# Kernel optimization log

Hardware: AMD Instinct MI355X
Metric: run time of the kernel (lower is better)

Reference implementation:

```python
import jax, jax.numpy as jnp
import numpy as np

N, T, F_IN, F_OUT, E = 20000, 4, 64, 64, 640000


def setup_inputs() -> dict:
    key = jax.random.key(0)
    k1, k2, k3, k4, k5, k6 = jax.random.split(key, 6)
    node_features = jax.random.normal(k1, (N, T, F_IN), dtype=jnp.float32)
    edge_weights = jax.random.uniform(k2, (T, E), dtype=jnp.float32)
    src = jax.random.randint(k3, (E,), 0, N, dtype=jnp.int32)
    dst = jax.random.randint(k4, (E,), 0, N, dtype=jnp.int32)
    W = jax.random.normal(k5, (F_OUT, F_IN), dtype=jnp.float32) / np.sqrt(F_IN)
    b = jax.random.normal(k6, (F_OUT,), dtype=jnp.float32) * 0.01
    return {"node_features": node_features, "edge_weights": edge_weights,
            "src": src, "dst": dst, "W": W, "b": b}


def reference(node_features, edge_weights, src, dst, W, b):
    # u_mul_e: gather source node features and scale by per-edge, per-time weight
    # edge_weights (T, E) -> transposed (E, T) -> broadcast over feature dim
    msg = node_features[src] * edge_weights.T[:, :, None]          # (E, T, F_IN)
    # fn.sum: scatter-sum messages into destination nodes
    h = jax.ops.segment_sum(msg, dst, num_segments=node_features.shape[0])  # (N, T, F_IN)
    # nn.Linear(in_features, out_features)
    return h @ W.T + b                                             # (N, T, F_OUT)
```

## Files before the change

kernel.cpp:

```cpp
#include <hip/hip_runtime.h>

#define N_NODES 20000
#define T_STEPS 4
#define F_DIM   64
#define E_EDGES 640000
#define ROWS    (N_NODES * T_STEPS)
#define ROW_ELEMS (T_STEPS * F_DIM)

#define SCATTER_BLOCKS   (E_EDGES / 1024)
#define TRANSFORM_BLOCKS (ROWS / 64)
#define OVF_CAP          4096

__device__ __forceinline__ unsigned short f32_to_bf16_rne(float f) {
    unsigned u = __float_as_uint(f);
    u += 0x7FFFu + ((u >> 16) & 1u);
    return (unsigned short)(u >> 16);
}
__device__ __forceinline__ float bf16_to_f32(unsigned short h) {
    return __uint_as_float((unsigned)h << 16);
}
__device__ __forceinline__ unsigned w_to_u12(float f) {
    unsigned q = __float2uint_rn(f * 4096.0f);
    return q > 4095u ? 4095u : q;
}

__global__ __launch_bounds__(256) void fused_build_kernel(
    const float* __restrict__ x, const float* __restrict__ W,
    unsigned short* __restrict__ yb,
    const int* __restrict__ src, const int* __restrict__ dst,
    const float* __restrict__ ew,
    int* __restrict__ cnt, uint2* __restrict__ buckets, int cap,
    int4* __restrict__ ovf, int* __restrict__ ovf_cnt)
{
    __shared__ float wt[64 * 64];

    if (blockIdx.x < SCATTER_BLOCKS) {
        const int base = blockIdx.x * 1024 + threadIdx.x;
#pragma unroll
        for (int j = 0; j < 4; ++j) {
            const int e = base + j * 256;
            const unsigned w0 = w_to_u12(ew[e]);
            const unsigned w1 = w_to_u12(ew[E_EDGES + e]);
            const unsigned w2 = w_to_u12(ew[2 * E_EDGES + e]);
            const unsigned w3 = w_to_u12(ew[3 * E_EDGES + e]);
            const unsigned s  = (unsigned)src[e];
            const unsigned lo = s | (w0 << 16) | (w1 << 28);
            const unsigned hi = (w1 >> 4) | (w2 << 8) | (w3 << 20);
            const int d = dst[e];
            const int pos = atomicAdd(&cnt[d], 1);
            if (pos < cap) {
                buckets[(size_t)d * cap + pos] = make_uint2(lo, hi);
            } else {
                const int o = atomicAdd(ovf_cnt, 1);
                if (o < OVF_CAP) { int4 r; r.x = (int)lo; r.y = (int)hi; r.z = d; r.w = 0; ovf[o] = r; }
            }
        }
        return;
    }

    const int tid  = threadIdx.x;
    const int row0 = (blockIdx.x - SCATTER_BLOCKS) * 64;

    {
        const int o  = tid & 63;
        const int fb = (tid >> 6) * 16;
#pragma unroll
        for (int k = 0; k < 16; ++k) {
            const int f = fb + k;
            wt[f * 64 + o] = W[o * 64 + f];
        }
    }
    __syncthreads();

    const int rg = tid >> 4;
    const int oq = (tid & 15) * 4;

    float acc[4][4];
#pragma unroll
    for (int i = 0; i < 4; ++i)
#pragma unroll
        for (int j = 0; j < 4; ++j) acc[i][j] = 0.0f;

    const float4* xg4 = (const float4*)(x + (size_t)(row0 + rg * 4) * 64);

#pragma unroll 4
    for (int fc = 0; fc < 16; ++fc) {
        float4 xv[4];
#pragma unroll
        for (int i = 0; i < 4; ++i) xv[i] = xg4[i * 16 + fc];
#pragma unroll
        for (int j = 0; j < 4; ++j) {
            const int f = fc * 4 + j;
            const float4 w4 = *(const float4*)&wt[f * 64 + oq];
            const float xj0 = j == 0 ? xv[0].x : j == 1 ? xv[0].y : j == 2 ? xv[0].z : xv[0].w;
            const float xj1 = j == 0 ? xv[1].x : j == 1 ? xv[1].y : j == 2 ? xv[1].z : xv[1].w;
            const float xj2 = j == 0 ? xv[2].x : j == 1 ? xv[2].y : j == 2 ? xv[2].z : xv[2].w;
            const float xj3 = j == 0 ? xv[3].x : j == 1 ? xv[3].y : j == 2 ? xv[3].z : xv[3].w;
            acc[0][0] += xj0 * w4.x; acc[0][1] += xj0 * w4.y; acc[0][2] += xj0 * w4.z; acc[0][3] += xj0 * w4.w;
            acc[1][0] += xj1 * w4.x; acc[1][1] += xj1 * w4.y; acc[1][2] += xj1 * w4.z; acc[1][3] += xj1 * w4.w;
            acc[2][0] += xj2 * w4.x; acc[2][1] += xj2 * w4.y; acc[2][2] += xj2 * w4.z; acc[2][3] += xj2 * w4.w;
            acc[3][0] += xj3 * w4.x; acc[3][1] += xj3 * w4.y; acc[3][2] += xj3 * w4.z; acc[3][3] += xj3 * w4.w;
        }
    }

#pragma unroll
    for (int i = 0; i < 4; ++i) {
        const int r = row0 + rg * 4 + i;
        ushort4 h;
        h.x = f32_to_bf16_rne(acc[i][0]);
        h.y = f32_to_bf16_rne(acc[i][1]);
        h.z = f32_to_bf16_rne(acc[i][2]);
        h.w = f32_to_bf16_rne(acc[i][3]);
        *(ushort4*)(yb + (size_t)r * 64 + oq) = h;
    }
}

__device__ __forceinline__ float dec_w(uint2 r, int t) {
    const unsigned long long pk = (unsigned long long)r.x |
                                  ((unsigned long long)r.y << 32);
    const unsigned q = (unsigned)(pk >> (16 + 12 * t)) & 0xFFFu;
    return (float)q * (1.0f / 4096.0f);
}

__global__ __launch_bounds__(256) void accumulate_kernel(
    const unsigned short* __restrict__ yb, const int* __restrict__ cnt,
    const uint2* __restrict__ buckets, int cap,
    const int4* __restrict__ ovf, const int* __restrict__ ovf_cnt,
    const float* __restrict__ b, float* __restrict__ out)
{
    const int lane = threadIdx.x & 63;
    const int n    = blockIdx.x * 4 + (threadIdx.x >> 6);
    const int t    = lane >> 4;
    const int l4   = lane * 4;

    int deg = cnt[n];
    if (deg > cap) deg = cap;
    const uint2* rp = buckets + (size_t)n * cap;

    float4 acc = make_float4(0.f, 0.f, 0.f, 0.f);

    int k = 0;
    for (; k + 16 <= deg; k += 16) {
        uint2 r[16];
#pragma unroll
        for (int i = 0; i < 16; ++i) r[i] = rp[k + i];
        ushort4 v[16];
#pragma unroll
        for (int i = 0; i < 16; ++i)
            v[i] = *(const ushort4*)(yb + (size_t)(r[i].x & 0xFFFFu) * ROW_ELEMS + l4);
#pragma unroll
        for (int i = 0; i < 16; ++i) {
            const float w = dec_w(r[i], t);
            acc.x += bf16_to_f32(v[i].x) * w;
            acc.y += bf16_to_f32(v[i].y) * w;
            acc.z += bf16_to_f32(v[i].z) * w;
            acc.w += bf16_to_f32(v[i].w) * w;
        }
    }
    for (; k + 4 <= deg; k += 4) {
        uint2 r[4];
#pragma unroll
        for (int i = 0; i < 4; ++i) r[i] = rp[k + i];
        ushort4 v[4];
#pragma unroll
        for (int i = 0; i < 4; ++i)
            v[i] = *(const ushort4*)(yb + (size_t)(r[i].x & 0xFFFFu) * ROW_ELEMS + l4);
#pragma unroll
        for (int i = 0; i < 4; ++i) {
            const float w = dec_w(r[i], t);
            acc.x += bf16_to_f32(v[i].x) * w;
            acc.y += bf16_to_f32(v[i].y) * w;
            acc.z += bf16_to_f32(v[i].z) * w;
            acc.w += bf16_to_f32(v[i].w) * w;
        }
    }
    for (; k < deg; ++k) {
        const uint2 r = rp[k];
        const float w = dec_w(r, t);
        const ushort4 v = *(const ushort4*)(yb + (size_t)(r.x & 0xFFFFu) * ROW_ELEMS + l4);
        acc.x += bf16_to_f32(v.x) * w;
        acc.y += bf16_to_f32(v.y) * w;
        acc.z += bf16_to_f32(v.z) * w;
        acc.w += bf16_to_f32(v.w) * w;
    }

    {
        int m = *ovf_cnt;
        if (m > OVF_CAP) m = OVF_CAP;
        for (int i = 0; i < m; ++i) {
            const int4 rr = ovf[i];
            if (rr.z == n) {
                const uint2 r = make_uint2((unsigned)rr.x, (unsigned)rr.y);
                const float w = dec_w(r, t);
                const ushort4 v = *(const ushort4*)(yb + (size_t)(r.x & 0xFFFFu) * ROW_ELEMS + l4);
                acc.x += bf16_to_f32(v.x) * w;
                acc.y += bf16_to_f32(v.y) * w;
                acc.z += bf16_to_f32(v.z) * w;
                acc.w += bf16_to_f32(v.w) * w;
            }
        }
    }

    const float4 bv = *(const float4*)(b + (lane & 15) * 4);
    acc.x += bv.x; acc.y += bv.y; acc.z += bv.z; acc.w += bv.w;
    *(float4*)(out + (size_t)n * ROW_ELEMS + l4) = acc;
}

extern "C" void kernel_launch(void* const* d_in, const int* in_sizes, int n_in,
                              void* d_out, int out_size, void* d_ws, size_t ws_size,
                              hipStream_t stream) {
    const float* x   = (const float*)d_in[0];
    const float* ew  = (const float*)d_in[1];
    const int*   src = (const int*)  d_in[2];
    const int*   dst = (const int*)  d_in[3];
    const float* W   = (const float*)d_in[4];
    const float* b   = (const float*)d_in[5];
    float*       out = (float*)d_out;

    char* ws = (char*)d_ws;
    size_t off = 0;
    auto alloc = [&](size_t bytes) {
        void* p = ws + off;
        off += (bytes + 255) & ~(size_t)255;
        return p;
    };
    unsigned short* yb  = (unsigned short*)alloc((size_t)ROWS * 64 * 2);
    int*            cnt = (int*) alloc((N_NODES + 1) * sizeof(int));
    int4*           ovf = (int4*)alloc((size_t)OVF_CAP * sizeof(int4));
    int*            ovf_cnt = cnt + N_NODES;

    size_t rem = (ws_size > off) ? (ws_size - off) : 0;
    int cap = (int)(rem / ((size_t)N_NODES * sizeof(uint2)));
    if (cap > 64) cap = 64;
    if (cap < 1) cap = 1;
    uint2* buckets = (uint2*)(ws + off);

    hipMemsetAsync(cnt, 0, (N_NODES + 1) * sizeof(int), stream);
    fused_build_kernel<<<SCATTER_BLOCKS + TRANSFORM_BLOCKS, 256, 0, stream>>>(
        x, W, yb, src, dst, ew, cnt, buckets, cap, ovf, ovf_cnt);
    accumulate_kernel<<<N_NODES / 4, 256, 0, stream>>>(
        yb, cnt, buckets, cap, ovf, ovf_cnt, b, out);
}
```

Measured before the change: 171.5 us.

## Split edge buckets and counters per XCC to localize atomics

The scatter phase reads the hardware XCC id and keeps a separate counter array and bucket region per XCC (8 regions of 16 slots each), so the atomicAdds on a destination counter come from a single die instead of contending across dies. The accumulate kernel reads the eight per-region degrees and walks each region's slots with fixed batches of four. Streaming inputs are now read with nontemporal loads, and the bucket capacity is fixed rather than sized from the workspace. The cost is an 8x larger counter memset, a larger and sparser bucket array with more scattered reads in accumulate, and a silent dependence on the workspace being big enough.

After: 188.0 us. +9.6%, slower.

```diff
diff --git a/kernel.cpp b/kernel.cpp
--- a/kernel.cpp
+++ b/kernel.cpp
@@ -11,6 +11,12 @@
 #define TRANSFORM_BLOCKS (ROWS / 64)
 #define OVF_CAP          4096
 
+#define NREG   8
+#define CAPR   16
+#define ROWSLOT (NREG * CAPR)
+
+typedef float f32x4 __attribute__((ext_vector_type(4)));
+
 __device__ __forceinline__ unsigned short f32_to_bf16_rne(float f) {
     unsigned u = __float_as_uint(f);
     u += 0x7FFFu + ((u >> 16) & 1u);
@@ -29,27 +35,32 @@
     unsigned short* __restrict__ yb,
     const int* __restrict__ src, const int* __restrict__ dst,
     const float* __restrict__ ew,
-    int* __restrict__ cnt, uint2* __restrict__ buckets, int cap,
+    int* __restrict__ cnt, uint2* __restrict__ buckets,
     int4* __restrict__ ovf, int* __restrict__ ovf_cnt)
 {
     __shared__ float wt[64 * 64];
 
     if (blockIdx.x < SCATTER_BLOCKS) {
+        unsigned xcc;
+        asm volatile("s_getreg_b32 %0, hwreg(HW_REG_XCC_ID)" : "=s"(xcc));
+        const int reg = (int)(xcc & 7u);
+        int* creg = cnt + (size_t)reg * N_NODES;
+
         const int base = blockIdx.x * 1024 + threadIdx.x;
 #pragma unroll
         for (int j = 0; j < 4; ++j) {
             const int e = base + j * 256;
-            const unsigned w0 = w_to_u12(ew[e]);
-            const unsigned w1 = w_to_u12(ew[E_EDGES + e]);
-            const unsigned w2 = w_to_u12(ew[2 * E_EDGES + e]);
-            const unsigned w3 = w_to_u12(ew[3 * E_EDGES + e]);
-            const unsigned s  = (unsigned)src[e];
+            const unsigned w0 = w_to_u12(__builtin_nontemporal_load(&ew[e]));
+            const unsigned w1 = w_to_u12(__builtin_nontemporal_load(&ew[E_EDGES + e]));
+            const unsigned w2 = w_to_u12(__builtin_nontemporal_load(&ew[2 * E_EDGES + e]));
+            const unsigned w3 = w_to_u12(__builtin_nontemporal_load(&ew[3 * E_EDGES + e]));
+            const unsigned s  = (unsigned)__builtin_nontemporal_load(&src[e]);
             const unsigned lo = s | (w0 << 16) | (w1 << 28);
             const unsigned hi = (w1 >> 4) | (w2 << 8) | (w3 << 20);
-            const int d = dst[e];
-            const int pos = atomicAdd(&cnt[d], 1);
-            if (pos < cap) {
-                buckets[(size_t)d * cap + pos] = make_uint2(lo, hi);
+            const int d = __builtin_nontemporal_load(&dst[e]);
+            const int pos = atomicAdd(&creg[d], 1);
+            if (pos < CAPR) {
+                buckets[(size_t)d * ROWSLOT + reg * CAPR + pos] = make_uint2(lo, hi);
             } else {
                 const int o = atomicAdd(ovf_cnt, 1);
                 if (o < OVF_CAP) { int4 r; r.x = (int)lo; r.y = (int)hi; r.z = d; r.w = 0; ovf[o] = r; }
@@ -81,21 +92,21 @@
 #pragma unroll
         for (int j = 0; j < 4; ++j) acc[i][j] = 0.0f;
 
-    const float4* xg4 = (const float4*)(x + (size_t)(row0 + rg * 4) * 64);
+    const f32x4* xg4 = (const f32x4*)(x + (size_t)(row0 + rg * 4) * 64);
 
 #pragma unroll 4
     for (int fc = 0; fc < 16; ++fc) {
-        float4 xv[4];
-#pragma unroll
-        for (int i = 0; i < 4; ++i) xv[i] = xg4[i * 16 + fc];
+        f32x4 xv[4];
+#pragma unroll
+        for (int i = 0; i < 4; ++i) xv[i] = __builtin_nontemporal_load(&xg4[i * 16 + fc]);
 #pragma unroll
         for (int j = 0; j < 4; ++j) {
             const int f = fc * 4 + j;
             const float4 w4 = *(const float4*)&wt[f * 64 + oq];
-            const float xj0 = j == 0 ? xv[0].x : j == 1 ? xv[0].y : j == 2 ? xv[0].z : xv[0].w;
-            const float xj1 = j == 0 ? xv[1].x : j == 1 ? xv[1].y : j == 2 ? xv[1].z : xv[1].w;
-            const float xj2 = j == 0 ? xv[2].x : j == 1 ? xv[2].y : j == 2 ? xv[2].z : xv[2].w;
-            const float xj3 = j == 0 ? xv[3].x : j == 1 ? xv[3].y : j == 2 ? xv[3].z : xv[3].w;
+            const float xj0 = xv[0][j];
+            const float xj1 = xv[1][j];
+            const float xj2 = xv[2][j];
+            const float xj3 = xv[3][j];
             acc[0][0] += xj0 * w4.x; acc[0][1] += xj0 * w4.y; acc[0][2] += xj0 * w4.z; acc[0][3] += xj0 * w4.w;
             acc[1][0] += xj1 * w4.x; acc[1][1] += xj1 * w4.y; acc[1][2] += xj1 * w4.z; acc[1][3] += xj1 * w4.w;
             acc[2][0] += xj2 * w4.x; acc[2][1] += xj2 * w4.y; acc[2][2] += xj2 * w4.z; acc[2][3] += xj2 * w4.w;
@@ -122,9 +133,32 @@
     return (float)q * (1.0f / 4096.0f);
 }
 
+#define BATCH4(RP, K0)                                                        \
+    {                                                                         \
+        const uint2 R0 = (RP)[(K0) + 0], R1 = (RP)[(K0) + 1],                 \
+                    R2 = (RP)[(K0) + 2], R3 = (RP)[(K0) + 3];                 \
+        const ushort4 V0 = *(const ushort4*)(yb + (size_t)(R0.x & 0xFFFFu) * ROW_ELEMS + l4); \
+        const ushort4 V1 = *(const ushort4*)(yb + (size_t)(R1.x & 0xFFFFu) * ROW_ELEMS + l4); \
+        const ushort4 V2 = *(const ushort4*)(yb + (size_t)(R2.x & 0xFFFFu) * ROW_ELEMS + l4); \
+        const ushort4 V3 = *(const ushort4*)(yb + (size_t)(R3.x & 0xFFFFu) * ROW_ELEMS + l4); \
+        float w;                                                              \
+        w = dec_w(R0, t);                                                     \
+        acc.x += bf16_to_f32(V0.x) * w; acc.y += bf16_to_f32(V0.y) * w;       \
+        acc.z += bf16_to_f32(V0.z) * w; acc.w += bf16_to_f32(V0.w) * w;       \
+        w = dec_w(R1, t);                                                     \
+        acc.x += bf16_to_f32(V1.x) * w; acc.y += bf16_to_f32(V1.y) * w;       \
+        acc.z += bf16_to_f32(V1.z) * w; acc.w += bf16_to_f32(V1.w) * w;       \
+        w = dec_w(R2, t);                                                     \
+        acc.x += bf16_to_f32(V2.x) * w; acc.y += bf16_to_f32(V2.y) * w;       \
+        acc.z += bf16_to_f32(V2.z) * w; acc.w += bf16_to_f32(V2.w) * w;       \
+        w = dec_w(R3, t);                                                     \
+        acc.x += bf16_to_f32(V3.x) * w; acc.y += bf16_to_f32(V3.y) * w;       \
+        acc.z += bf16_to_f32(V3.z) * w; acc.w += bf16_to_f32(V3.w) * w;       \
+    }
+
 __global__ __launch_bounds__(256) void accumulate_kernel(
     const unsigned short* __restrict__ yb, const int* __restrict__ cnt,
-    const uint2* __restrict__ buckets, int cap,
+    const uint2* __restrict__ buckets,
     const int4* __restrict__ ovf, const int* __restrict__ ovf_cnt,
     const float* __restrict__ b, float* __restrict__ out)
 {
@@ -133,55 +167,34 @@
     const int t    = lane >> 4;
     const int l4   = lane * 4;
 
-    int deg = cnt[n];
-    if (deg > cap) deg = cap;
-    const uint2* rp = buckets + (size_t)n * cap;
-
+    int degc[NREG];
+#pragma unroll
+    for (int r = 0; r < NREG; ++r) {
+        int d = cnt[(size_t)r * N_NODES + n];
+        degc[r] = d > CAPR ? CAPR : d;
+    }
+
+    const uint2* rowp = buckets + (size_t)n * ROWSLOT;
     float4 acc = make_float4(0.f, 0.f, 0.f, 0.f);
 
-    int k = 0;
-    for (; k + 16 <= deg; k += 16) {
-        uint2 r[16];
-#pragma unroll
-        for (int i = 0; i < 16; ++i) r[i] = rp[k + i];
-        ushort4 v[16];
-#pragma unroll
-        for (int i = 0; i < 16; ++i)
-            v[i] = *(const ushort4*)(yb + (size_t)(r[i].x & 0xFFFFu) * ROW_ELEMS + l4);
-#pragma unroll
-        for (int i = 0; i < 16; ++i) {
-            const float w = dec_w(r[i], t);
-            acc.x += bf16_to_f32(v[i].x) * w;
-            acc.y += bf16_to_f32(v[i].y) * w;
-            acc.z += bf16_to_f32(v[i].z) * w;
-            acc.w += bf16_to_f32(v[i].w) * w;
-        }
-    }
-    for (; k + 4 <= deg; k += 4) {
-        uint2 r[4];
-#pragma unroll
-        for (int i = 0; i < 4; ++i) r[i] = rp[k + i];
-        ushort4 v[4];
-#pragma unroll
-        for (int i = 0; i < 4; ++i)
-            v[i] = *(const ushort4*)(yb + (size_t)(r[i].x & 0xFFFFu) * ROW_ELEMS + l4);
-#pragma unroll
-        for (int i = 0; i < 4; ++i) {
-            const float w = dec_w(r[i], t);
-            acc.x += bf16_to_f32(v[i].x) * w;
-            acc.y += bf16_to_f32(v[i].y) * w;
-            acc.z += bf16_to_f32(v[i].z) * w;
-            acc.w += bf16_to_f32(v[i].w) * w;
-        }
-    }
-    for (; k < deg; ++k) {
-        const uint2 r = rp[k];
-        const float w = dec_w(r, t);
-        const ushort4 v = *(const ushort4*)(yb + (size_t)(r.x & 0xFFFFu) * ROW_ELEMS + l4);
-        acc.x += bf16_to_f32(v.x) * w;
-        acc.y += bf16_to_f32(v.y) * w;
-        acc.z += bf16_to_f32(v.z) * w;
-        acc.w += bf16_to_f32(v.w) * w;
+#pragma unroll
+    for (int r = 0; r < NREG; ++r) {
+        const uint2* rp = rowp + r * CAPR;
+        const int d = degc[r];
+        int k = 0;
+        if (d >= 4)  { BATCH4(rp, 0);  k = 4;
+        if (d >= 8)  { BATCH4(rp, 4);  k = 8;
+        if (d >= 12) { BATCH4(rp, 8);  k = 12;
+        if (d >= 16) { BATCH4(rp, 12); k = 16; } } } }
+        for (; k < d; ++k) {
+            const uint2 rr = rp[k];
+            const float w = dec_w(rr, t);
+            const ushort4 v = *(const ushort4*)(yb + (size_t)(rr.x & 0xFFFFu) * ROW_ELEMS + l4);
+            acc.x += bf16_to_f32(v.x) * w;
+            acc.y += bf16_to_f32(v.y) * w;
+            acc.z += bf16_to_f32(v.z) * w;
+            acc.w += bf16_to_f32(v.w) * w;
+        }
     }
 
     {
@@ -190,9 +203,9 @@
         for (int i = 0; i < m; ++i) {
             const int4 rr = ovf[i];
             if (rr.z == n) {
-                const uint2 r = make_uint2((unsigned)rr.x, (unsigned)rr.y);
-                const float w = dec_w(r, t);
-                const ushort4 v = *(const ushort4*)(yb + (size_t)(r.x & 0xFFFFu) * ROW_ELEMS + l4);
+                const uint2 r2 = make_uint2((unsigned)rr.x, (unsigned)rr.y);
+                const float w = dec_w(r2, t);
+                const ushort4 v = *(const ushort4*)(yb + (size_t)(r2.x & 0xFFFFu) * ROW_ELEMS + l4);
                 acc.x += bf16_to_f32(v.x) * w;
                 acc.y += bf16_to_f32(v.y) * w;
                 acc.z += bf16_to_f32(v.z) * w;
@@ -225,19 +238,16 @@
         return p;
     };
     unsigned short* yb  = (unsigned short*)alloc((size_t)ROWS * 64 * 2);
-    int*            cnt = (int*) alloc((N_NODES + 1) * sizeof(int));
+    int*            cnt = (int*) alloc(((size_t)NREG * N_NODES + 1) * sizeof(int));
     int4*           ovf = (int4*)alloc((size_t)OVF_CAP * sizeof(int4));
-    int*            ovf_cnt = cnt + N_NODES;
-
-    size_t rem = (ws_size > off) ? (ws_size - off) : 0;
-    int cap = (int)(rem / ((size_t)N_NODES * sizeof(uint2)));
-    if (cap > 64) cap = 64;
-    if (cap < 1) cap = 1;
-    uint2* buckets = (uint2*)(ws + off);
-
-    hipMemsetAsync(cnt, 0, (N_NODES + 1) * sizeof(int), stream);
+    uint2*          buckets = (uint2*)alloc((size_t)N_NODES * ROWSLOT * sizeof(uint2));
+    int*            ovf_cnt = cnt + (size_t)NREG * N_NODES;
+    (void)ws_size;
+
+    hipError_t err = hipMemsetAsync(cnt, 0, ((size_t)NREG * N_NODES + 1) * sizeof(int), stream);
+    (void)err;
     fused_build_kernel<<<SCATTER_BLOCKS + TRANSFORM_BLOCKS, 256, 0, stream>>>(
-        x, W, yb, src, dst, ew, cnt, buckets, cap, ovf, ovf_cnt);
+        x, W, yb, src, dst, ew, cnt, buckets, ovf, ovf_cnt);
     accumulate_kernel<<<N_NODES / 4, 256, 0, stream>>>(
-        yb, cnt, buckets, cap, ovf, ovf_cnt, b, out);
-}
+        yb, cnt, buckets, ovf, ovf_cnt, b, out);
+}
```
